# Performance work log

Hardware: AMD Instinct MI355X
Metric: run time of the kernel (lower is better)

## Reference

```python
import jax, jax.numpy as jnp
import numpy as np

NG, NPG, NF = 256, 64, 64          # graphs, nodes/graph, features (NPG == NF: x is per-graph [N,N])
HC, NL = 504, 4                     # hidden_channels, num_layers (HC*NL == TRIU)
E_PER = 1024                        # edges per graph
ALPHA = 0.5
EPS = 1e-5
TRIU = NF * (NF - 1) // 2           # 2016 strict-upper-triangle entries
HIDDEN, NCLS = 1024, 2


def _bn(x, g, b):
    # BatchNorm1d in training mode: biased batch statistics
    m = x.mean(0)
    v = x.var(0)
    return (x - m) * jax.lax.rsqrt(v + EPS) * g + b


def _gcn(x, src, dst, W, b):
    n = x.shape[0]
    xw = x @ W
    deg = jax.ops.segment_sum(jnp.ones(src.shape[0], x.dtype), dst, num_segments=n) + 1.0
    dinv = jax.lax.rsqrt(deg)
    coef = (dinv[src] * dinv[dst])[:, None]
    agg = jax.ops.segment_sum(xw[src] * coef, dst, num_segments=n)
    return agg + xw * (dinv * dinv)[:, None] + b


def _pool(x, batch):
    # global_mean_pool; every graph has exactly NPG nodes
    return jax.ops.segment_sum(x, batch, num_segments=NG) / NPG


def setup_inputs():
    key = jax.random.key(0)
    ks = jax.random.split(key, 16)
    total = NG * NPG
    x = jax.random.normal(ks[0], (total, NF), jnp.float32)
    offs = (jnp.arange(NG) * NPG)[:, None]
    edge_src = (jax.random.randint(ks[1], (NG, E_PER), 0, NPG) + offs).reshape(-1)
    edge_dst = (jax.random.randint(ks[2], (NG, E_PER), 0, NPG) + offs).reshape(-1)
    batch = jnp.arange(total) // NPG

    def lin(k, fi, fo):
        return jax.random.normal(k, (fi, fo), jnp.float32) / np.sqrt(fi)

    Wg0 = lin(ks[3], NF, HC)
    bg0 = jnp.zeros((HC,), jnp.float32)
    Wg_rest = jax.random.normal(ks[4], (NL - 1, HC, HC), jnp.float32) / np.sqrt(HC)
    bg_rest = jnp.zeros((NL - 1, HC), jnp.float32)
    gx = jnp.ones((TRIU,), jnp.float32); bx = jnp.zeros((TRIU,), jnp.float32)
    gh = jnp.ones((HC * NL,), jnp.float32); bh = jnp.zeros((HC * NL,), jnp.float32)
    Watt = lin(ks[5], TRIU, 1); batt = jnp.zeros((1,), jnp.float32)
    D1 = TRIU + HC * NL  # 4032
    Wm1 = lin(ks[6], D1, HIDDEN); bm1 = jnp.zeros((HIDDEN,), jnp.float32)
    gm1 = jnp.ones((HIDDEN,), jnp.float32); bem1 = jnp.zeros((HIDDEN,), jnp.float32)
    Wm2 = lin(ks[7], HIDDEN, HIDDEN // 2); bm2 = jnp.zeros((HIDDEN // 2,), jnp.float32)
    gm2 = jnp.ones((HIDDEN // 2,), jnp.float32); bem2 = jnp.zeros((HIDDEN // 2,), jnp.float32)
    Wm3 = lin(ks[8], HIDDEN // 2, HIDDEN // 2); bm3 = jnp.zeros((HIDDEN // 2,), jnp.float32)
    gm3 = jnp.ones((HIDDEN // 2,), jnp.float32); bem3 = jnp.zeros((HIDDEN // 2,), jnp.float32)
    Wm4 = lin(ks[9], HIDDEN // 2, NCLS); bm4 = jnp.zeros((NCLS,), jnp.float32)
    return dict(x=x, Wg0=Wg0, bg0=bg0, Wg_rest=Wg_rest, bg_rest=bg_rest, gx=gx, bx=bx,
                gh=gh, bh=bh, Watt=Watt, batt=batt, Wm1=Wm1, bm1=bm1, gm1=gm1, bem1=bem1,
                Wm2=Wm2, bm2=bm2, gm2=gm2, bem2=bem2, Wm3=Wm3, bm3=bm3, gm3=gm3, bem3=bem3,
                Wm4=Wm4, bm4=bm4, edge_src=edge_src, edge_dst=edge_dst, batch=batch)


def reference(x, Wg0, bg0, Wg_rest, bg_rest, gx, bx, gh, bh, Watt, batt,
              Wm1, bm1, gm1, bem1, Wm2, bm2, gm2, bem2, Wm3, bm3, gm3, bem3,
              Wm4, bm4, edge_src, edge_dst, batch):
    # stacked GCN convs (no nonlinearity between convs, as in source)
    cur = _gcn(x, edge_src, edge_dst, Wg0, bg0)
    hs = [_pool(cur, batch)]
    for i in range(NL - 1):
        cur = _gcn(cur, edge_src, edge_dst, Wg_rest[i], bg_rest[i])
        hs.append(_pool(cur, batch))
    h = _bn(jnp.concatenate(hs, axis=1), gh, bh)          # [NG, HC*NL]
    # per-graph strict upper triangle of the [N,N] input matrix (== triu().nonzero() trick)
    iu, ju = jnp.triu_indices(NF, k=1)
    xv = x.reshape(NG, NPG, NF)[:, iu, ju]                # [NG, TRIU]
    xv = _bn(xv, gx, bx)
    att = jax.nn.sigmoid(xv @ Watt + batt)                # [NG, 1]
    xf = att * xv + (1.0 - att) * h * ALPHA               # attention-weighted fusion
    z = jnp.concatenate([xf, h], axis=1)                  # [NG, TRIU + HC*NL]
    z = jax.nn.relu(_bn(z @ Wm1 + bm1, gm1, bem1))
    z = jax.nn.relu(_bn(z @ Wm2 + bm2, gm2, bem2))
    z = jax.nn.relu(_bn(z @ Wm3 + bm3, gm3, bem3))
    return z @ Wm4 + bm4                                   # [NG, NCLS]
```

## Files before the change

kernel.cpp:

```cpp
#include <hip/hip_runtime.h>
#include <math.h>

#define NGRAPH 256
#define NPG 64
#define NFEAT 64
#define HC 504
#define NLAY 4
#define EPER 1024
#define NTRIU 2016
#define DCAT 4032
#define HID1 1024
#define HID2 512

#define GCN_LDS (65536 + 73728 + 16384)

typedef __attribute__((ext_vector_type(8))) short bfrag8;
typedef __attribute__((ext_vector_type(4))) float f32x4;

struct __align__(8) us4 { unsigned short a, b, c, d; };

__device__ __forceinline__ unsigned short f2b(float f) {
    union { float f; unsigned u; } v; v.f = f;
    unsigned r = (v.u + 0x7fffu + ((v.u >> 16) & 1u)) >> 16;
    return (unsigned short)r;
}
__device__ __forceinline__ float b2f(unsigned short h) {
    union { unsigned u; float f; } v; v.u = ((unsigned)h) << 16;
    return v.f;
}

__global__ void triu_off(int* __restrict__ off)
{
    int i = threadIdx.x;
    if (i >= 63) return;
    int o = 63 * i - i * (i - 1) / 2;
    for (int j = i + 1; j < 64; ++j) { off[o] = i * 64 + j; ++o; }
}

__global__ void convWt(const float* __restrict__ W, unsigned short* __restrict__ Wt,
                       int K, int N, int KP, long long sStride, long long dStride)
{
    W  += (size_t)blockIdx.z * sStride;
    Wt += (size_t)blockIdx.z * dStride;
    __shared__ float T[32][33];
    int k0 = blockIdx.y * 32, n0 = blockIdx.x * 32;
    int tx = threadIdx.x, ty = threadIdx.y;
#pragma unroll
    for (int j = 0; j < 32; j += 8) {
        int k = k0 + ty + j, n = n0 + tx;
        T[ty + j][tx] = (k < K && n < N) ? W[(size_t)k * N + n] : 0.f;
    }
    __syncthreads();
#pragma unroll
    for (int j = 0; j < 32; j += 8) {
        int n = n0 + ty + j, k = k0 + tx;
        Wt[(size_t)n * KP + k] = f2b(T[tx][ty + j]);
    }
}

__global__ void convW4(const float* __restrict__ W, unsigned short* __restrict__ W4,
                       int K, int N, int KL, long long sStride, long long dStride)
{
    W  += (size_t)blockIdx.z * sStride;
    W4 += (size_t)blockIdx.z * dStride;
    __shared__ float T[32][33];
    int k0 = blockIdx.y * 32, n0 = blockIdx.x * 32;
    int tx = threadIdx.x, ty = threadIdx.y;
#pragma unroll
    for (int j = 0; j < 32; j += 8) {
        int k = k0 + ty + j, n = n0 + tx;
        T[ty + j][tx] = (k < K && n < N) ? W[(size_t)k * N + n] : 0.f;
    }
    __syncthreads();
#pragma unroll
    for (int j = 0; j < 32; j += 8) {
        int n = n0 + ty + j, k = k0 + tx;
        int idx = ((n >> 4) * (KL >> 5) + (k >> 5)) * 512
                + (((k >> 3) & 3) << 7) + ((n & 15) << 3) + (k & 7);
        W4[idx] = f2b(T[tx][ty + j]);
    }
}

template<int KL>
__device__ __forceinline__ void gcn_layer(const unsigned short* __restrict__ W4,
                                          const float* __restrict__ bias,
                                          unsigned short* cur, unsigned short* xwt,
                                          const unsigned short* ahl,
                                          float* __restrict__ hsg,
                                          int wv, int lm, int lh)
{
    constexpr int KTS = KL >> 5;
    const int colw = wv << 6;
    const int kswz = (lm & 7) << 3;
    const int lane8 = ((lh << 4) + lm) << 3;

    float bv[4];
#pragma unroll
    for (int cc = 0; cc < 4; ++cc) {
        int c = colw + cc * 16 + lm;
        bv[cc] = (c < HC) ? bias[c] : 0.f;
    }

    f32x4 acc[4][4];
#pragma unroll
    for (int m0 = 0; m0 < 4; ++m0)
#pragma unroll
        for (int cc = 0; cc < 4; ++cc) acc[m0][cc] = (f32x4){0.f, 0.f, 0.f, 0.f};

    bfrag8 bq[2][4];
#pragma unroll
    for (int cc = 0; cc < 4; ++cc)
        bq[0][cc] = *(const bfrag8*)(const void*)&W4[(size_t)((wv * 4 + cc) * KTS + 0) * 512 + lane8];
    if (KTS > 1) {
#pragma unroll
        for (int cc = 0; cc < 4; ++cc)
            bq[1][cc] = *(const bfrag8*)(const void*)&W4[(size_t)((wv * 4 + cc) * KTS + 1) * 512 + lane8];
    }
#pragma unroll
    for (int kt = 0; kt < KTS; ++kt) {
        bfrag8 a[4];
#pragma unroll
        for (int m0 = 0; m0 < 4; ++m0)
            a[m0] = *(const bfrag8*)(const void*)&cur[(m0 * 16 + lm) * 512 + ((kt * 32 + (lh << 3)) ^ kswz)];
        bfrag8 bc[4];
#pragma unroll
        for (int cc = 0; cc < 4; ++cc) bc[cc] = bq[kt & 1][cc];
        if (kt + 2 < KTS) {
#pragma unroll
            for (int cc = 0; cc < 4; ++cc)
                bq[kt & 1][cc] = *(const bfrag8*)(const void*)&W4[(size_t)((wv * 4 + cc) * KTS + kt + 2) * 512 + lane8];
        }
#pragma unroll
        for (int cc = 0; cc < 4; ++cc)
#pragma unroll
            for (int m0 = 0; m0 < 4; ++m0)
                acc[m0][cc] = __builtin_amdgcn_mfma_f32_16x16x32_bf16(a[m0], bc[cc], acc[m0][cc], 0, 0, 0);
    }
    __syncthreads();

#pragma unroll
    for (int cc = 0; cc < 4; ++cc) {
        const int c = colw + cc * 16 + lm;
#pragma unroll
        for (int m0 = 0; m0 < 4; ++m0) {
            const int rloc = m0 * 16 + (lh << 2);
            us4 p;
            p.a = f2b(acc[m0][cc][0]); p.b = f2b(acc[m0][cc][1]);
            p.c = f2b(acc[m0][cc][2]); p.d = f2b(acc[m0][cc][3]);
            *(us4*)(void*)&xwt[c * 72 + rloc] = p;
        }
    }

    bfrag8 ahf[4][2], alf[4][2];
#pragma unroll
    for (int m0 = 0; m0 < 4; ++m0)
#pragma unroll
        for (int kc = 0; kc < 2; ++kc) {
            int o = (m0 * 16 + lm) * 64 + kc * 32 + (lh << 3);
            ahf[m0][kc] = *(const bfrag8*)(const void*)&ahl[o];
            alf[m0][kc] = *(const bfrag8*)(const void*)&ahl[4096 + o];
        }
#pragma unroll
    for (int m0 = 0; m0 < 4; ++m0)
#pragma unroll
        for (int cc = 0; cc < 4; ++cc) acc[m0][cc] = (f32x4){0.f, 0.f, 0.f, 0.f};
#pragma unroll
    for (int cc = 0; cc < 4; ++cc) {
        const int c = colw + cc * 16 + lm;
        bfrag8 b0 = *(const bfrag8*)(const void*)&xwt[c * 72 + (lh << 3)];
        bfrag8 b1 = *(const bfrag8*)(const void*)&xwt[c * 72 + 32 + (lh << 3)];
#pragma unroll
        for (int m0 = 0; m0 < 4; ++m0) {
            acc[m0][cc] = __builtin_amdgcn_mfma_f32_16x16x32_bf16(ahf[m0][0], b0, acc[m0][cc], 0, 0, 0);
            acc[m0][cc] = __builtin_amdgcn_mfma_f32_16x16x32_bf16(alf[m0][0], b0, acc[m0][cc], 0, 0, 0);
            acc[m0][cc] = __builtin_amdgcn_mfma_f32_16x16x32_bf16(ahf[m0][1], b1, acc[m0][cc], 0, 0, 0);
            acc[m0][cc] = __builtin_amdgcn_mfma_f32_16x16x32_bf16(alf[m0][1], b1, acc[m0][cc], 0, 0, 0);
        }
    }

#pragma unroll
    for (int cc = 0; cc < 4; ++cc) {
        const int c = colw + cc * 16 + lm;
        float cs = 0.f;
#pragma unroll
        for (int m0 = 0; m0 < 4; ++m0) {
            const int rb = m0 * 16 + (lh << 2);
#pragma unroll
            for (int r = 0; r < 4; ++r) {
                float v = acc[m0][cc][r] + bv[cc];
                cs += v;
                const int row = rb + r;
                cur[row * 512 + (c ^ ((row & 7) << 3))] = f2b(v);
            }
        }
        cs += __shfl_xor(cs, 16, 64);
        cs += __shfl_xor(cs, 32, 64);
        if (lh == 0 && c < HC) hsg[c] = cs * (1.0f / 64.0f);
    }
    __syncthreads();
}

__global__ __launch_bounds__(512, 2) void gcn_all(const float* __restrict__ x,
                                                  const int* __restrict__ esrc,
                                                  const int* __restrict__ edst,
                                                  const unsigned short* __restrict__ Wt0,
                                                  const unsigned short* __restrict__ Wt123,
                                                  const float* __restrict__ bg0,
                                                  const float* __restrict__ bgR,
                                                  float* __restrict__ hs)
{
    extern __shared__ char lds[];
    unsigned short* cur = (unsigned short*)lds;
    unsigned short* xwt = (unsigned short*)(lds + 65536);
    unsigned short* ahl = (unsigned short*)(lds + 65536 + 73728);
    float* Af   = (float*)(lds + 65536);
    int*   cnt  = (int*)(lds + 65536 + 16384);
    float* dinv = (float*)(lds + 65536 + 16384 + 256);

    const int g = blockIdx.x, tid = threadIdx.x;
    const int wv = tid >> 6, lane = tid & 63;
    const int lm = lane & 15, lh = lane >> 4;

    for (int i = tid; i < 4096; i += 512) Af[i] = 0.f;
    if (tid < 64) cnt[tid] = 0;
    __syncthreads();
    for (int e = tid; e < EPER; e += 512)
        atomicAdd(&cnt[edst[(size_t)g * EPER + e] & 63], 1);
    __syncthreads();
    if (tid < 64) dinv[tid] = rsqrtf((float)cnt[tid] + 1.0f);
    __syncthreads();
    for (int e = tid; e < EPER; e += 512) {
        int s = esrc[(size_t)g * EPER + e] & 63;
        int d = edst[(size_t)g * EPER + e] & 63;
        atomicAdd(&Af[d * 64 + s], dinv[s] * dinv[d]);
    }
    __syncthreads();
    if (tid < 64) Af[tid * 64 + tid] += dinv[tid] * dinv[tid];
    __syncthreads();
    for (int i = tid; i < 4096; i += 512) {
        float v = Af[i];
        unsigned short h = f2b(v);
        ahl[i] = h;
        ahl[4096 + i] = f2b(v - b2f(h));
    }
    for (int i = tid; i < 1024; i += 512) {
        float4 v = ((const float4*)(x + (size_t)g * 4096))[i];
        int row = (i * 4) >> 6, col = (i * 4) & 63;
        unsigned short* p = &cur[row * 512 + (col ^ ((row & 7) << 3))];
        p[0] = f2b(v.x); p[1] = f2b(v.y); p[2] = f2b(v.z); p[3] = f2b(v.w);
    }
    __syncthreads();

    float* hsg = hs + (size_t)g * (HC * NLAY);
    gcn_layer<64>(Wt0, bg0, cur, xwt, ahl, hsg, wv, lm, lh);
    for (int l = 1; l < NLAY; ++l)
        gcn_layer<512>(Wt123 + (size_t)(l - 1) * 262144, bgR + (l - 1) * HC,
                       cur, xwt, ahl, hsg + l * HC, wv, lm, lh);
}

__global__ __launch_bounds__(256) void stats_part(const float* __restrict__ in,
                                                  float* __restrict__ ps,
                                                  float* __restrict__ pss,
                                                  int F, int rpb)
{
    int f = blockIdx.x * 256 + threadIdx.x;
    if (f >= F) return;
    int r0 = blockIdx.y * rpb;
    float s = 0.f, ss = 0.f;
    for (int r = r0; r < r0 + rpb; ++r) {
        float v = in[(size_t)r * F + f];
        s += v; ss += v * v;
    }
    ps [(size_t)blockIdx.y * F + f] = s;
    pss[(size_t)blockIdx.y * F + f] = ss;
}

__global__ __launch_bounds__(256) void stats_fin(const float* __restrict__ ps,
                                                 const float* __restrict__ pss,
                                                 float* __restrict__ mean,
                                                 float* __restrict__ inv,
                                                 int F, int GB, float invR)
{
    int f = blockIdx.x * 256 + threadIdx.x;
    if (f >= F) return;
    float s = 0.f, ss = 0.f;
    for (int b = 0; b < GB; ++b) { s += ps[(size_t)b * F + f]; ss += pss[(size_t)b * F + f]; }
    float m = s * invR;
    mean[f] = m;
    inv[f]  = rsqrtf(ss * invR - m * m + 1e-5f);
}

__global__ __launch_bounds__(256) void xv_gather(const float* __restrict__ x,
                                                 const int* __restrict__ off,
                                                 float* __restrict__ xv,
                                                 float* __restrict__ ps,
                                                 float* __restrict__ pss)
{
    int t = blockIdx.x * 256 + threadIdx.x;
    if (t >= NTRIU) return;
    int o = off[t];
    int g0 = blockIdx.y * 16;
    float s = 0.f, ss = 0.f;
    for (int g = g0; g < g0 + 16; ++g) {
        float v = x[(size_t)g * 4096 + o];
        xv[(size_t)g * NTRIU + t] = v;
        s += v; ss += v * v;
    }
    ps [(size_t)blockIdx.y * NTRIU + t] = s;
    pss[(size_t)blockIdx.y * NTRIU + t] = ss;
}

__global__ __launch_bounds__(256) void attz_fused(const float* __restrict__ xv,
                                                  const float* __restrict__ xm,
                                                  const float* __restrict__ xi,
                                                  const float* __restrict__ gx,
                                                  const float* __restrict__ bx,
                                                  const float* __restrict__ hsrc,
                                                  const float* __restrict__ hm,
                                                  const float* __restrict__ hi,
                                                  const float* __restrict__ gh,
                                                  const float* __restrict__ bh,
                                                  const float* __restrict__ Watt,
                                                  const float* __restrict__ batt,
                                                  unsigned short* __restrict__ zhi,
                                                  unsigned short* __restrict__ zlo)
{
    int g = blockIdx.x;
    __shared__ float xs[NTRIU];
    __shared__ float red[256];
    float s = 0.f;
    for (int t = threadIdx.x; t < NTRIU; t += 256) {
        float v = (xv[(size_t)g * NTRIU + t] - xm[t]) * xi[t] * gx[t] + bx[t];
        xs[t] = v;
        s += v * Watt[t];
    }
    red[threadIdx.x] = s;
    __syncthreads();
    for (int w = 128; w > 0; w >>= 1) {
        if (threadIdx.x < w) red[threadIdx.x] += red[threadIdx.x + w];
        __syncthreads();
    }
    float att = 1.0f / (1.0f + expf(-(red[0] + batt[0])));
    for (int t = threadIdx.x; t < NTRIU; t += 256) {
        float hn = (hsrc[(size_t)g * NTRIU + t] - hm[t]) * hi[t] * gh[t] + bh[t];
        float zf = att * xs[t] + (1.0f - att) * hn * 0.5f;
        unsigned short h0 = f2b(zf);
        zhi[(size_t)g * DCAT + t] = h0;
        zlo[(size_t)g * DCAT + t] = f2b(zf - b2f(h0));
        unsigned short h1 = f2b(hn);
        zhi[(size_t)g * DCAT + NTRIU + t] = h1;
        zlo[(size_t)g * DCAT + NTRIU + t] = f2b(hn - b2f(h1));
    }
}

__global__ __launch_bounds__(256) void gemm_bf_sk(const unsigned short* __restrict__ Ahi,
                                                  const unsigned short* __restrict__ Alo,
                                                  const unsigned short* __restrict__ Bt,
                                                  float* __restrict__ P,
                                                  int N, int K, int chunk)
{
    __shared__ unsigned short Ah[2][2048], Al[2][2048], Bs[2][2048];
    const int tid  = threadIdx.x;
    const int wave = tid >> 6, lane = tid & 63;
    const int row0 = blockIdx.y << 6, col0 = blockIdx.x << 6;
    const int kb = blockIdx.z * chunk;
    const int NT = chunk >> 5;
    const int sr = tid >> 2, sk = (tid & 3) << 3;
    const unsigned short* gAh = Ahi + (size_t)(row0 + sr) * K + kb + sk;
    const unsigned short* gAl = Alo + (size_t)(row0 + sr) * K + kb + sk;
    const unsigned short* gB  = Bt  + (size_t)(col0 + sr) * K + kb + sk;

    int4 rh = *(const int4*)(const void*)gAh;
    int4 rl = *(const int4*)(const void*)gAl;
    int4 rb = *(const int4*)(const void*)gB;
    *(int4*)(void*)&Ah[0][tid << 3] = rh;
    *(int4*)(void*)&Al[0][tid << 3] = rl;
    *(int4*)(void*)&Bs[0][tid << 3] = rb;
    __syncthreads();

    f32x4 acc0 = {0.f, 0.f, 0.f, 0.f};
    f32x4 acc1 = acc0, acc2 = acc0, acc3 = acc0;
    const int aoff = (wave * 16 + (lane & 15)) * 32 + ((lane >> 4) << 3);
    const int boff = (lane & 15) * 32 + ((lane >> 4) << 3);

    for (int t = 0; t < NT; ++t) {
        if (t + 1 < NT) {
            rh = *(const int4*)(const void*)(gAh + (t + 1) * 32);
            rl = *(const int4*)(const void*)(gAl + (t + 1) * 32);
            rb = *(const int4*)(const void*)(gB  + (t + 1) * 32);
        }
        const unsigned short* ah = Ah[t & 1];
        const unsigned short* al = Al[t & 1];
        const unsigned short* bs = Bs[t & 1];
        bfrag8 a  = *(const bfrag8*)(const void*)&ah[aoff];
        bfrag8 a2 = *(const bfrag8*)(const void*)&al[aoff];
        bfrag8 b0 = *(const bfrag8*)(const void*)&bs[boff];
        bfrag8 b1 = *(const bfrag8*)(const void*)&bs[boff + 16 * 32];
        bfrag8 b2 = *(const bfrag8*)(const void*)&bs[boff + 32 * 32];
        bfrag8 b3 = *(const bfrag8*)(const void*)&bs[boff + 48 * 32];
        acc0 = __builtin_amdgcn_mfma_f32_16x16x32_bf16(a,  b0, acc0, 0, 0, 0);
        acc0 = __builtin_amdgcn_mfma_f32_16x16x32_bf16(a2, b0, acc0, 0, 0, 0);
        acc1 = __builtin_amdgcn_mfma_f32_16x16x32_bf16(a,  b1, acc1, 0, 0, 0);
        acc1 = __builtin_amdgcn_mfma_f32_16x16x32_bf16(a2, b1, acc1, 0, 0, 0);
        acc2 = __builtin_amdgcn_mfma_f32_16x16x32_bf16(a,  b2, acc2, 0, 0, 0);
        acc2 = __builtin_amdgcn_mfma_f32_16x16x32_bf16(a2, b2, acc2, 0, 0, 0);
        acc3 = __builtin_amdgcn_mfma_f32_16x16x32_bf16(a,  b3, acc3, 0, 0, 0);
        acc3 = __builtin_amdgcn_mfma_f32_16x16x32_bf16(a2, b3, acc3, 0, 0, 0);
        if (t + 1 < NT) {
            *(int4*)(void*)&Ah[(t + 1) & 1][tid << 3] = rh;
            *(int4*)(void*)&Al[(t + 1) & 1][tid << 3] = rl;
            *(int4*)(void*)&Bs[(t + 1) & 1][tid << 3] = rb;
        }
        __syncthreads();
    }

    float* Pp = P + (size_t)blockIdx.z * NGRAPH * N;
    const int rbase = row0 + wave * 16 + ((lane >> 4) << 2);
    const int cbase = col0 + (lane & 15);
#pragma unroll
    for (int r = 0; r < 4; ++r) {
        int grow = rbase + r;
        Pp[(size_t)grow * N + cbase +  0] = acc0[r];
        Pp[(size_t)grow * N + cbase + 16] = acc1[r];
        Pp[(size_t)grow * N + cbase + 32] = acc2[r];
        Pp[(size_t)grow * N + cbase + 48] = acc3[r];
    }
}

__global__ __launch_bounds__(256) void reduce_add(const float* __restrict__ P,
                                                  const float* __restrict__ bias,
                                                  float* __restrict__ C, int MN,
                                                  int Nmask, int S)
{
    int i = blockIdx.x * 256 + threadIdx.x;
    if (i >= MN) return;
    float s = 0.f;
    for (int t = 0; t < S; ++t) s += P[(size_t)t * MN + i];
    C[i] = s + bias[i & Nmask];
}

__global__ __launch_bounds__(256) void bn_apply_bf(const float* __restrict__ M_,
                                                   const float* __restrict__ mean,
                                                   const float* __restrict__ inv,
                                                   const float* __restrict__ gamma,
                                                   const float* __restrict__ beta,
                                                   unsigned short* __restrict__ hi,
                                                   unsigned short* __restrict__ lo,
                                                   int total, int mask)
{
    int i = blockIdx.x * 256 + threadIdx.x;
    if (i >= total) return;
    int f = i & mask;
    float v = (M_[i] - mean[f]) * inv[f] * gamma[f] + beta[f];
    v = fmaxf(v, 0.f);
    unsigned short h = f2b(v);
    hi[i] = h;
    lo[i] = f2b(v - b2f(h));
}

__global__ __launch_bounds__(256) void final_kernel(const unsigned short* __restrict__ Xhi,
                                                    const unsigned short* __restrict__ Xlo,
                                                    const float* __restrict__ W,
                                                    const float* __restrict__ b,
                                                    float* __restrict__ out)
{
    int g = blockIdx.x;
    float s0 = 0.f, s1 = 0.f;
    for (int k = threadIdx.x; k < HID2; k += 256) {
        float v = b2f(Xhi[(size_t)g * HID2 + k]) + b2f(Xlo[(size_t)g * HID2 + k]);
        s0 += v * W[k * 2 + 0];
        s1 += v * W[k * 2 + 1];
    }
    __shared__ float r0[256], r1[256];
    r0[threadIdx.x] = s0; r1[threadIdx.x] = s1;
    __syncthreads();
    for (int w = 128; w > 0; w >>= 1) {
        if (threadIdx.x < w) {
            r0[threadIdx.x] += r0[threadIdx.x + w];
            r1[threadIdx.x] += r1[threadIdx.x + w];
        }
        __syncthreads();
    }
    if (threadIdx.x == 0) {
        out[g * 2 + 0] = r0[0] + b[0];
        out[g * 2 + 1] = r1[0] + b[1];
    }
}

extern "C" void kernel_launch(void* const* d_in, const int* in_sizes, int n_in,
                              void* d_out, int out_size, void* d_ws, size_t ws_size,
                              hipStream_t stream)
{
    const float* x      = (const float*)d_in[0];
    const float* Wg0    = (const float*)d_in[1];
    const float* bg0    = (const float*)d_in[2];
    const float* WgR    = (const float*)d_in[3];
    const float* bgR    = (const float*)d_in[4];
    const float* gx     = (const float*)d_in[5];
    const float* bx     = (const float*)d_in[6];
    const float* gh     = (const float*)d_in[7];
    const float* bh     = (const float*)d_in[8];
    const float* Watt   = (const float*)d_in[9];
    const float* batt   = (const float*)d_in[10];
    const float* Wm1    = (const float*)d_in[11];
    const float* bm1    = (const float*)d_in[12];
    const float* gm1    = (const float*)d_in[13];
    const float* bem1   = (const float*)d_in[14];
    const float* Wm2    = (const float*)d_in[15];
    const float* bm2    = (const float*)d_in[16];
    const float* gm2    = (const float*)d_in[17];
    const float* bem2   = (const float*)d_in[18];
    const float* Wm3    = (const float*)d_in[19];
    const float* bm3    = (const float*)d_in[20];
    const float* gm3    = (const float*)d_in[21];
    const float* bem3   = (const float*)d_in[22];
    const float* Wm4    = (const float*)d_in[23];
    const float* bm4    = (const float*)d_in[24];
    const int*   esrc   = (const int*)d_in[25];
    const int*   edst   = (const int*)d_in[26];
    float* out = (float*)d_out;

    char* w = (char*)d_ws;
    auto alloc = [&](size_t bytes) -> char* {
        char* p = w;
        w += (bytes + 255) & ~(size_t)255;
        return p;
    };
    unsigned short* Wt0   = (unsigned short*)alloc((size_t)512 * 64 * 2);
    unsigned short* Wt123 = (unsigned short*)alloc((size_t)3 * 512 * 512 * 2);
    unsigned short* W1t   = (unsigned short*)alloc((size_t)HID1 * DCAT * 2);
    unsigned short* W2t   = (unsigned short*)alloc((size_t)HID2 * HID1 * 2);
    unsigned short* W3t   = (unsigned short*)alloc((size_t)HID2 * HID2 * 2);
    float*          hs    = (float*)alloc((size_t)NGRAPH * NTRIU * 4);
    float*          xv    = (float*)alloc((size_t)NGRAPH * NTRIU * 4);
    unsigned short* zhi   = (unsigned short*)alloc((size_t)NGRAPH * DCAT * 2);
    unsigned short* zlo   = (unsigned short*)alloc((size_t)NGRAPH * DCAT * 2);
    float*          P     = (float*)alloc((size_t)8 * NGRAPH * HID1 * 4);
    float*          mf    = (float*)alloc((size_t)NGRAPH * HID1 * 4);
    unsigned short* m1hi  = (unsigned short*)alloc((size_t)NGRAPH * HID1 * 2);
    unsigned short* m1lo  = (unsigned short*)alloc((size_t)NGRAPH * HID1 * 2);
    unsigned short* m2hi  = (unsigned short*)alloc((size_t)NGRAPH * HID2 * 2);
    unsigned short* m2lo  = (unsigned short*)alloc((size_t)NGRAPH * HID2 * 2);
    unsigned short* m3hi  = (unsigned short*)alloc((size_t)NGRAPH * HID2 * 2);
    unsigned short* m3lo  = (unsigned short*)alloc((size_t)NGRAPH * HID2 * 2);
    float*          ps    = (float*)alloc((size_t)16 * NTRIU * 4);
    float*          pss   = (float*)alloc((size_t)16 * NTRIU * 4);
    float*          xm    = (float*)alloc(NTRIU * 4);
    float*          xi    = (float*)alloc(NTRIU * 4);
    float*          hm    = (float*)alloc(NTRIU * 4);
    float*          hiv   = (float*)alloc(NTRIU * 4);
    float*          mmean = (float*)alloc(HID1 * 4);
    float*          minv  = (float*)alloc(HID1 * 4);
    int*            off   = (int*)alloc(NTRIU * 4);

    hipFuncSetAttribute((const void*)gcn_all,
                        hipFuncAttributeMaxDynamicSharedMemorySize, GCN_LDS);

    triu_off<<<1, 64, 0, stream>>>(off);
    convW4<<<dim3(16, 2, 1),   dim3(32, 8), 0, stream>>>(Wg0, Wt0, 64, HC, 64, 0, 0);
    convW4<<<dim3(16, 16, 3),  dim3(32, 8), 0, stream>>>(WgR, Wt123, HC, HC, 512,
                                                         (long long)HC * HC, 512LL * 512);
    convWt<<<dim3(32, 126, 1), dim3(32, 8), 0, stream>>>(Wm1, W1t, DCAT, HID1, DCAT, 0, 0);
    convWt<<<dim3(16, 32, 1),  dim3(32, 8), 0, stream>>>(Wm2, W2t, HID1, HID2, HID1, 0, 0);
    convWt<<<dim3(16, 16, 1),  dim3(32, 8), 0, stream>>>(Wm3, W3t, HID2, HID2, HID2, 0, 0);

    gcn_all<<<NGRAPH, 512, GCN_LDS, stream>>>(x, esrc, edst, Wt0, Wt123, bg0, bgR, hs);

    stats_part<<<dim3(8, 16), 256, 0, stream>>>(hs, ps, pss, NTRIU, 16);
    stats_fin<<<8, 256, 0, stream>>>(ps, pss, hm, hiv, NTRIU, 16, 1.0f / NGRAPH);
    xv_gather<<<dim3(8, 16), 256, 0, stream>>>(x, off, xv, ps, pss);
    stats_fin<<<8, 256, 0, stream>>>(ps, pss, xm, xi, NTRIU, 16, 1.0f / NGRAPH);
    attz_fused<<<NGRAPH, 256, 0, stream>>>(xv, xm, xi, gx, bx, hs, hm, hiv, gh, bh,
                                           Watt, batt, zhi, zlo);

    gemm_bf_sk<<<dim3(16, 4, 7), 256, 0, stream>>>(zhi, zlo, W1t, P, HID1, DCAT, 576);
    reduce_add<<<1024, 256, 0, stream>>>(P, bm1, mf, NGRAPH * HID1, HID1 - 1, 7);
    stats_part<<<dim3(4, 16), 256, 0, stream>>>(mf, ps, pss, HID1, 16);
    stats_fin<<<4, 256, 0, stream>>>(ps, pss, mmean, minv, HID1, 16, 1.0f / NGRAPH);
    bn_apply_bf<<<1024, 256, 0, stream>>>(mf, mmean, minv, gm1, bem1, m1hi, m1lo,
                                          NGRAPH * HID1, HID1 - 1);

    gemm_bf_sk<<<dim3(8, 4, 8), 256, 0, stream>>>(m1hi, m1lo, W2t, P, HID2, HID1, 128);
    reduce_add<<<512, 256, 0, stream>>>(P, bm2, mf, NGRAPH * HID2, HID2 - 1, 8);
    stats_part<<<dim3(2, 16), 256, 0, stream>>>(mf, ps, pss, HID2, 16);
    stats_fin<<<2, 256, 0, stream>>>(ps, pss, mmean, minv, HID2, 16, 1.0f / NGRAPH);
    bn_apply_bf<<<512, 256, 0, stream>>>(mf, mmean, minv, gm2, bem2, m2hi, m2lo,
                                         NGRAPH * HID2, HID2 - 1);

    gemm_bf_sk<<<dim3(8, 4, 8), 256, 0, stream>>>(m2hi, m2lo, W3t, P, HID2, HID2, 64);
    reduce_add<<<512, 256, 0, stream>>>(P, bm3, mf, NGRAPH * HID2, HID2 - 1, 8);
    stats_part<<<dim3(2, 16), 256, 0, stream>>>(mf, ps, pss, HID2, 16);
    stats_fin<<<2, 256, 0, stream>>>(ps, pss, mmean, minv, HID2, 16, 1.0f / NGRAPH);
    bn_apply_bf<<<512, 256, 0, stream>>>(mf, mmean, minv, gm3, bem3, m3hi, m3lo,
                                         NGRAPH * HID2, HID2 - 1);

    final_kernel<<<NGRAPH, 256, 0, stream>>>(m3hi, m3lo, Wm4, bm4, out);
}
```

Measured before the change: 175.9 us.

## Widen GCN block to 1024 threads, fuse split-K reduce with BN stats, drop triu kernel

The per-graph GCN kernel now runs 1024 threads (16 waves), each owning 32 output columns instead of 64. The aggregation GEMM is transposed so results are written to LDS as packed 4-wide stores, and pooled sums are reduced with shuffles and float4 writes. Separately, the split-K reduction is fused with the BatchNorm partial-statistics pass, which removes one kernel and one read of the intermediate per MLP layer. The triu offset kernel is replaced by closed-form index math inside xv_gather. The wider block halves the per-wave register footprint but adds more waves competing for LDS and barriers, and the fused reduce uses fewer, larger blocks.

```diff
diff --git a/kernel.cpp b/kernel.cpp
--- a/kernel.cpp
+++ b/kernel.cpp
@@ -29,14 +29,6 @@
     return v.f;
 }
 
-__global__ void triu_off(int* __restrict__ off)
-{
-    int i = threadIdx.x;
-    if (i >= 63) return;
-    int o = 63 * i - i * (i - 1) / 2;
-    for (int j = i + 1; j < 64; ++j) { off[o] = i * 64 + j; ++o; }
-}
-
 __global__ void convWt(const float* __restrict__ W, unsigned short* __restrict__ Wt,
                        int K, int N, int KP, long long sStride, long long dStride)
 {
@@ -90,31 +82,24 @@
                                           int wv, int lm, int lh)
 {
     constexpr int KTS = KL >> 5;
-    const int colw = wv << 6;
+    const int colw = wv << 5;
     const int kswz = (lm & 7) << 3;
     const int lane8 = ((lh << 4) + lm) << 3;
 
-    float bv[4];
-#pragma unroll
-    for (int cc = 0; cc < 4; ++cc) {
-        int c = colw + cc * 16 + lm;
-        bv[cc] = (c < HC) ? bias[c] : 0.f;
-    }
-
-    f32x4 acc[4][4];
+    f32x4 acc[4][2];
 #pragma unroll
     for (int m0 = 0; m0 < 4; ++m0)
 #pragma unroll
-        for (int cc = 0; cc < 4; ++cc) acc[m0][cc] = (f32x4){0.f, 0.f, 0.f, 0.f};
-
-    bfrag8 bq[2][4];
-#pragma unroll
-    for (int cc = 0; cc < 4; ++cc)
-        bq[0][cc] = *(const bfrag8*)(const void*)&W4[(size_t)((wv * 4 + cc) * KTS + 0) * 512 + lane8];
+        for (int cc = 0; cc < 2; ++cc) acc[m0][cc] = (f32x4){0.f, 0.f, 0.f, 0.f};
+
+    bfrag8 bq[2][2];
+#pragma unroll
+    for (int cc = 0; cc < 2; ++cc)
+        bq[0][cc] = *(const bfrag8*)(const void*)&W4[(size_t)((wv * 2 + cc) * KTS + 0) * 512 + lane8];
     if (KTS > 1) {
 #pragma unroll
-        for (int cc = 0; cc < 4; ++cc)
-            bq[1][cc] = *(const bfrag8*)(const void*)&W4[(size_t)((wv * 4 + cc) * KTS + 1) * 512 + lane8];
+        for (int cc = 0; cc < 2; ++cc)
+            bq[1][cc] = *(const bfrag8*)(const void*)&W4[(size_t)((wv * 2 + cc) * KTS + 1) * 512 + lane8];
     }
 #pragma unroll
     for (int kt = 0; kt < KTS; ++kt) {
@@ -122,16 +107,15 @@
 #pragma unroll
         for (int m0 = 0; m0 < 4; ++m0)
             a[m0] = *(const bfrag8*)(const void*)&cur[(m0 * 16 + lm) * 512 + ((kt * 32 + (lh << 3)) ^ kswz)];
-        bfrag8 bc[4];
-#pragma unroll
-        for (int cc = 0; cc < 4; ++cc) bc[cc] = bq[kt & 1][cc];
+        bfrag8 bc[2];
+        bc[0] = bq[kt & 1][0]; bc[1] = bq[kt & 1][1];
         if (kt + 2 < KTS) {
 #pragma unroll
-            for (int cc = 0; cc < 4; ++cc)
-                bq[kt & 1][cc] = *(const bfrag8*)(const void*)&W4[(size_t)((wv * 4 + cc) * KTS + kt + 2) * 512 + lane8];
-        }
-#pragma unroll
-        for (int cc = 0; cc < 4; ++cc)
+            for (int cc = 0; cc < 2; ++cc)
+                bq[kt & 1][cc] = *(const bfrag8*)(const void*)&W4[(size_t)((wv * 2 + cc) * KTS + kt + 2) * 512 + lane8];
+        }
+#pragma unroll
+        for (int cc = 0; cc < 2; ++cc)
 #pragma unroll
             for (int m0 = 0; m0 < 4; ++m0)
                 acc[m0][cc] = __builtin_amdgcn_mfma_f32_16x16x32_bf16(a[m0], bc[cc], acc[m0][cc], 0, 0, 0);
@@ -139,75 +123,85 @@
     __syncthreads();
 
 #pragma unroll
-    for (int cc = 0; cc < 4; ++cc) {
+    for (int cc = 0; cc < 2; ++cc) {
         const int c = colw + cc * 16 + lm;
 #pragma unroll
         for (int m0 = 0; m0 < 4; ++m0) {
-            const int rloc = m0 * 16 + (lh << 2);
             us4 p;
             p.a = f2b(acc[m0][cc][0]); p.b = f2b(acc[m0][cc][1]);
             p.c = f2b(acc[m0][cc][2]); p.d = f2b(acc[m0][cc][3]);
-            *(us4*)(void*)&xwt[c * 72 + rloc] = p;
-        }
-    }
-
-    bfrag8 ahf[4][2], alf[4][2];
-#pragma unroll
-    for (int m0 = 0; m0 < 4; ++m0)
-#pragma unroll
-        for (int kc = 0; kc < 2; ++kc) {
-            int o = (m0 * 16 + lm) * 64 + kc * 32 + (lh << 3);
-            ahf[m0][kc] = *(const bfrag8*)(const void*)&ahl[o];
-            alf[m0][kc] = *(const bfrag8*)(const void*)&ahl[4096 + o];
-        }
-#pragma unroll
-    for (int m0 = 0; m0 < 4; ++m0)
-#pragma unroll
-        for (int cc = 0; cc < 4; ++cc) acc[m0][cc] = (f32x4){0.f, 0.f, 0.f, 0.f};
-#pragma unroll
-    for (int cc = 0; cc < 4; ++cc) {
-        const int c = colw + cc * 16 + lm;
-        bfrag8 b0 = *(const bfrag8*)(const void*)&xwt[c * 72 + (lh << 3)];
-        bfrag8 b1 = *(const bfrag8*)(const void*)&xwt[c * 72 + 32 + (lh << 3)];
-#pragma unroll
-        for (int m0 = 0; m0 < 4; ++m0) {
-            acc[m0][cc] = __builtin_amdgcn_mfma_f32_16x16x32_bf16(ahf[m0][0], b0, acc[m0][cc], 0, 0, 0);
-            acc[m0][cc] = __builtin_amdgcn_mfma_f32_16x16x32_bf16(alf[m0][0], b0, acc[m0][cc], 0, 0, 0);
-            acc[m0][cc] = __builtin_amdgcn_mfma_f32_16x16x32_bf16(ahf[m0][1], b1, acc[m0][cc], 0, 0, 0);
-            acc[m0][cc] = __builtin_amdgcn_mfma_f32_16x16x32_bf16(alf[m0][1], b1, acc[m0][cc], 0, 0, 0);
-        }
-    }
-
-#pragma unroll
-    for (int cc = 0; cc < 4; ++cc) {
-        const int c = colw + cc * 16 + lm;
-        float cs = 0.f;
-#pragma unroll
-        for (int m0 = 0; m0 < 4; ++m0) {
-            const int rb = m0 * 16 + (lh << 2);
-#pragma unroll
-            for (int r = 0; r < 4; ++r) {
-                float v = acc[m0][cc][r] + bv[cc];
-                cs += v;
-                const int row = rb + r;
-                cur[row * 512 + (c ^ ((row & 7) << 3))] = f2b(v);
-            }
-        }
-        cs += __shfl_xor(cs, 16, 64);
-        cs += __shfl_xor(cs, 32, 64);
-        if (lh == 0 && c < HC) hsg[c] = cs * (1.0f / 64.0f);
-    }
-    __syncthreads();
-}
-
-__global__ __launch_bounds__(512, 2) void gcn_all(const float* __restrict__ x,
-                                                  const int* __restrict__ esrc,
-                                                  const int* __restrict__ edst,
-                                                  const unsigned short* __restrict__ Wt0,
-                                                  const unsigned short* __restrict__ Wt123,
-                                                  const float* __restrict__ bg0,
-                                                  const float* __restrict__ bgR,
-                                                  float* __restrict__ hs)
+            *(us4*)(void*)&xwt[c * 72 + m0 * 16 + (lh << 2)] = p;
+        }
+    }
+
+    f32x4 acc2[2][4];
+#pragma unroll
+    for (int cc = 0; cc < 2; ++cc)
+#pragma unroll
+        for (int n0 = 0; n0 < 4; ++n0) acc2[cc][n0] = (f32x4){0.f, 0.f, 0.f, 0.f};
+#pragma unroll
+    for (int n0 = 0; n0 < 4; ++n0) {
+        const int o = (n0 * 16 + lm) * 64 + (lh << 3);
+        bfrag8 bh0 = *(const bfrag8*)(const void*)&ahl[o];
+        bfrag8 bh1 = *(const bfrag8*)(const void*)&ahl[o + 32];
+        bfrag8 bl0 = *(const bfrag8*)(const void*)&ahl[4096 + o];
+        bfrag8 bl1 = *(const bfrag8*)(const void*)&ahl[4096 + o + 32];
+#pragma unroll
+        for (int cc = 0; cc < 2; ++cc) {
+            const int c = colw + cc * 16 + lm;
+            bfrag8 a0 = *(const bfrag8*)(const void*)&xwt[c * 72 + (lh << 3)];
+            bfrag8 a1 = *(const bfrag8*)(const void*)&xwt[c * 72 + 32 + (lh << 3)];
+            acc2[cc][n0] = __builtin_amdgcn_mfma_f32_16x16x32_bf16(a0, bh0, acc2[cc][n0], 0, 0, 0);
+            acc2[cc][n0] = __builtin_amdgcn_mfma_f32_16x16x32_bf16(a0, bl0, acc2[cc][n0], 0, 0, 0);
+            acc2[cc][n0] = __builtin_amdgcn_mfma_f32_16x16x32_bf16(a1, bh1, acc2[cc][n0], 0, 0, 0);
+            acc2[cc][n0] = __builtin_amdgcn_mfma_f32_16x16x32_bf16(a1, bl1, acc2[cc][n0], 0, 0, 0);
+        }
+    }
+
+#pragma unroll
+    for (int cc = 0; cc < 2; ++cc) {
+        const int cb = colw + cc * 16 + (lh << 2);
+        float bv[4];
+#pragma unroll
+        for (int r = 0; r < 4; ++r) {
+            int c = cb + r;
+            bv[r] = (c < HC) ? bias[c] : 0.f;
+        }
+        float t0 = 0.f, t1 = 0.f, t2 = 0.f, t3 = 0.f;
+#pragma unroll
+        for (int n0 = 0; n0 < 4; ++n0) {
+            const int d = n0 * 16 + lm;
+            float v0 = acc2[cc][n0][0] + bv[0];
+            float v1 = acc2[cc][n0][1] + bv[1];
+            float v2 = acc2[cc][n0][2] + bv[2];
+            float v3 = acc2[cc][n0][3] + bv[3];
+            t0 += v0; t1 += v1; t2 += v2; t3 += v3;
+            us4 p;
+            p.a = f2b(v0); p.b = f2b(v1); p.c = f2b(v2); p.d = f2b(v3);
+            *(us4*)(void*)&cur[d * 512 + (cb ^ ((d & 7) << 3))] = p;
+        }
+#pragma unroll
+        for (int m = 1; m < 16; m <<= 1) {
+            t0 += __shfl_xor(t0, m, 64);
+            t1 += __shfl_xor(t1, m, 64);
+            t2 += __shfl_xor(t2, m, 64);
+            t3 += __shfl_xor(t3, m, 64);
+        }
+        if (lm == 0 && cb < HC)
+            *(float4*)&hsg[cb] = make_float4(t0 * (1.0f / 64.0f), t1 * (1.0f / 64.0f),
+                                             t2 * (1.0f / 64.0f), t3 * (1.0f / 64.0f));
+    }
+    __syncthreads();
+}
+
+__global__ __launch_bounds__(1024, 4) void gcn_all(const float* __restrict__ x,
+                                                   const int* __restrict__ esrc,
+                                                   const int* __restrict__ edst,
+                                                   const unsigned short* __restrict__ Wt0,
+                                                   const unsigned short* __restrict__ Wt123,
+                                                   const float* __restrict__ bg0,
+                                                   const float* __restrict__ bgR,
+                                                   float* __restrict__ hs)
 {
     extern __shared__ char lds[];
     unsigned short* cur = (unsigned short*)lds;
@@ -221,31 +215,30 @@
     const int wv = tid >> 6, lane = tid & 63;
     const int lm = lane & 15, lh = lane >> 4;
 
-    for (int i = tid; i < 4096; i += 512) Af[i] = 0.f;
+    for (int i = tid; i < 4096; i += 1024) Af[i] = 0.f;
     if (tid < 64) cnt[tid] = 0;
     __syncthreads();
-    for (int e = tid; e < EPER; e += 512)
-        atomicAdd(&cnt[edst[(size_t)g * EPER + e] & 63], 1);
+    atomicAdd(&cnt[edst[(size_t)g * EPER + tid] & 63], 1);
     __syncthreads();
     if (tid < 64) dinv[tid] = rsqrtf((float)cnt[tid] + 1.0f);
     __syncthreads();
-    for (int e = tid; e < EPER; e += 512) {
-        int s = esrc[(size_t)g * EPER + e] & 63;
-        int d = edst[(size_t)g * EPER + e] & 63;
+    {
+        int s = esrc[(size_t)g * EPER + tid] & 63;
+        int d = edst[(size_t)g * EPER + tid] & 63;
         atomicAdd(&Af[d * 64 + s], dinv[s] * dinv[d]);
     }
     __syncthreads();
     if (tid < 64) Af[tid * 64 + tid] += dinv[tid] * dinv[tid];
     __syncthreads();
-    for (int i = tid; i < 4096; i += 512) {
+    for (int i = tid; i < 4096; i += 1024) {
         float v = Af[i];
         unsigned short h = f2b(v);
         ahl[i] = h;
         ahl[4096 + i] = f2b(v - b2f(h));
     }
-    for (int i = tid; i < 1024; i += 512) {
-        float4 v = ((const float4*)(x + (size_t)g * 4096))[i];
-        int row = (i * 4) >> 6, col = (i * 4) & 63;
+    {
+        float4 v = ((const float4*)(x + (size_t)g * 4096))[tid];
+        int row = (tid * 4) >> 6, col = (tid * 4) & 63;
         unsigned short* p = &cur[row * 512 + (col ^ ((row & 7) << 3))];
         p[0] = f2b(v.x); p[1] = f2b(v.y); p[2] = f2b(v.z); p[3] = f2b(v.w);
     }
@@ -291,14 +284,17 @@
 }
 
 __global__ __launch_bounds__(256) void xv_gather(const float* __restrict__ x,
-                                                 const int* __restrict__ off,
                                                  float* __restrict__ xv,
                                                  float* __restrict__ ps,
                                                  float* __restrict__ pss)
 {
     int t = blockIdx.x * 256 + threadIdx.x;
     if (t >= NTRIU) return;
-    int o = off[t];
+    int i = (int)(63.5f - sqrtf(63.5f * 63.5f - 2.0f * (float)t));
+    while (63 * (i + 1) - (i + 1) * i / 2 <= t) ++i;
+    while (63 * i - i * (i - 1) / 2 > t) --i;
+    int j = t - (63 * i - i * (i - 1) / 2) + i + 1;
+    int o = i * 64 + j;
     int g0 = blockIdx.y * 16;
     float s = 0.f, ss = 0.f;
     for (int g = g0; g < g0 + 16; ++g) {
@@ -427,16 +423,27 @@
     }
 }
 
-__global__ __launch_bounds__(256) void reduce_add(const float* __restrict__ P,
-                                                  const float* __restrict__ bias,
-                                                  float* __restrict__ C, int MN,
-                                                  int Nmask, int S)
-{
-    int i = blockIdx.x * 256 + threadIdx.x;
-    if (i >= MN) return;
-    float s = 0.f;
-    for (int t = 0; t < S; ++t) s += P[(size_t)t * MN + i];
-    C[i] = s + bias[i & Nmask];
+__global__ __launch_bounds__(256) void reduce_stats(const float* __restrict__ P,
+                                                    const float* __restrict__ bias,
+                                                    float* __restrict__ mf,
+                                                    float* __restrict__ ps,
+                                                    float* __restrict__ pss,
+                                                    int N, int S)
+{
+    int f = blockIdx.x * 256 + threadIdx.x;
+    int r0 = blockIdx.y * 8;
+    size_t MN = (size_t)NGRAPH * N;
+    float bv = bias[f];
+    float s = 0.f, ss = 0.f;
+    for (int r = r0; r < r0 + 8; ++r) {
+        float v = 0.f;
+        for (int t = 0; t < S; ++t) v += P[(size_t)t * MN + (size_t)r * N + f];
+        v += bv;
+        mf[(size_t)r * N + f] = v;
+        s += v; ss += v * v;
+    }
+    ps [(size_t)blockIdx.y * N + f] = s;
+    pss[(size_t)blockIdx.y * N + f] = ss;
 }
 
 __global__ __launch_bounds__(256) void bn_apply_bf(const float* __restrict__ M_,
@@ -543,20 +550,18 @@
     unsigned short* m2lo  = (unsigned short*)alloc((size_t)NGRAPH * HID2 * 2);
     unsigned short* m3hi  = (unsigned short*)alloc((size_t)NGRAPH * HID2 * 2);
     unsigned short* m3lo  = (unsigned short*)alloc((size_t)NGRAPH * HID2 * 2);
-    float*          ps    = (float*)alloc((size_t)16 * NTRIU * 4);
-    float*          pss   = (float*)alloc((size_t)16 * NTRIU * 4);
+    float*          ps    = (float*)alloc((size_t)32 * NTRIU * 4);
+    float*          pss   = (float*)alloc((size_t)32 * NTRIU * 4);
     float*          xm    = (float*)alloc(NTRIU * 4);
     float*          xi    = (float*)alloc(NTRIU * 4);
     float*          hm    = (float*)alloc(NTRIU * 4);
     float*          hiv   = (float*)alloc(NTRIU * 4);
     float*          mmean = (float*)alloc(HID1 * 4);
     float*          minv  = (float*)alloc(HID1 * 4);
-    int*            off   = (int*)alloc(NTRIU * 4);
 
     hipFuncSetAttribute((const void*)gcn_all,
                         hipFuncAttributeMaxDynamicSharedMemorySize, GCN_LDS);
 
-    triu_off<<<1, 64, 0, stream>>>(off);
     convW4<<<dim3(16, 2, 1),   dim3(32, 8), 0, stream>>>(Wg0, Wt0, 64, HC, 64, 0, 0);
     convW4<<<dim3(16, 16, 3),  dim3(32, 8), 0, stream>>>(WgR, Wt123, HC, HC, 512,
                                                          (long long)HC * HC, 512LL * 512);
@@ -564,33 +569,30 @@
     convWt<<<dim3(16, 32, 1),  dim3(32, 8), 0, stream>>>(Wm2, W2t, HID1, HID2, HID1, 0, 0);
     convWt<<<dim3(16, 16, 1),  dim3(32, 8), 0, stream>>>(Wm3, W3t, HID2, HID2, HID2, 0, 0);
 
-    gcn_all<<<NGRAPH, 512, GCN_LDS, stream>>>(x, esrc, edst, Wt0, Wt123, bg0, bgR, hs);
+    gcn_all<<<NGRAPH, 1024, GCN_LDS, stream>>>(x, esrc, edst, Wt0, Wt123, bg0, bgR, hs);
 
     stats_part<<<dim3(8, 16), 256, 0, stream>>>(hs, ps, pss, NTRIU, 16);
     stats_fin<<<8, 256, 0, stream>>>(ps, pss, hm, hiv, NTRIU, 16, 1.0f / NGRAPH);
-    xv_gather<<<dim3(8, 16), 256, 0, stream>>>(x, off, xv, ps, pss);
+    xv_gather<<<dim3(8, 16), 256, 0, stream>>>(x, xv, ps, pss);
     stats_fin<<<8, 256, 0, stream>>>(ps, pss, xm, xi, NTRIU, 16, 1.0f / NGRAPH);
     attz_fused<<<NGRAPH, 256, 0, stream>>>(xv, xm, xi, gx, bx, hs, hm, hiv, gh, bh,
                                            Watt, batt, zhi, zlo);
 
     gemm_bf_sk<<<dim3(16, 4, 7), 256, 0, stream>>>(zhi, zlo, W1t, P, HID1, DCAT, 576);
-    reduce_add<<<1024, 256, 0, stream>>>(P, bm1, mf, NGRAPH * HID1, HID1 - 1, 7);
-    stats_part<<<dim3(4, 16), 256, 0, stream>>>(mf, ps, pss, HID1, 16);
-    stats_fin<<<4, 256, 0, stream>>>(ps, pss, mmean, minv, HID1, 16, 1.0f / NGRAPH);
+    reduce_stats<<<dim3(4, 32), 256, 0, stream>>>(P, bm1, mf, ps, pss, HID1, 7);
+    stats_fin<<<4, 256, 0, stream>>>(ps, pss, mmean, minv, HID1, 32, 1.0f / NGRAPH);
     bn_apply_bf<<<1024, 256, 0, stream>>>(mf, mmean, minv, gm1, bem1, m1hi, m1lo,
                                           NGRAPH * HID1, HID1 - 1);
 
     gemm_bf_sk<<<dim3(8, 4, 8), 256, 0, stream>>>(m1hi, m1lo, W2t, P, HID2, HID1, 128);
-    reduce_add<<<512, 256, 0, stream>>>(P, bm2, mf, NGRAPH * HID2, HID2 - 1, 8);
-    stats_part<<<dim3(2, 16), 256, 0, stream>>>(mf, ps, pss, HID2, 16);
-    stats_fin<<<2, 256, 0, stream>>>(ps, pss, mmean, minv, HID2, 16, 1.0f / NGRAPH);
+    reduce_stats<<<dim3(2, 32), 256, 0, stream>>>(P, bm2, mf, ps, pss, HID2, 8);
+    stats_fin<<<2, 256, 0, stream>>>(ps, pss, mmean, minv, HID2, 32, 1.0f / NGRAPH);
     bn_apply_bf<<<512, 256, 0, stream>>>(mf, mmean, minv, gm2, bem2, m2hi, m2lo,
                                          NGRAPH * HID2, HID2 - 1);
 
     gemm_bf_sk<<<dim3(8, 4, 8), 256, 0, stream>>>(m2hi, m2lo, W3t, P, HID2, HID2, 64);
-    reduce_add<<<512, 256, 0, stream>>>(P, bm3, mf, NGRAPH * HID2, HID2 - 1, 8);
-    stats_part<<<dim3(2, 16), 256, 0, stream>>>(mf, ps, pss, HID2, 16);
-    stats_fin<<<2, 256, 0, stream>>>(ps, pss, mmean, minv, HID2, 16, 1.0f / NGRAPH);
+    reduce_stats<<<dim3(2, 32), 256, 0, stream>>>(P, bm3, mf, ps, pss, HID2, 8);
+    stats_fin<<<2, 256, 0, stream>>>(ps, pss, mmean, minv, HID2, 32, 1.0f / NGRAPH);
     bn_apply_bf<<<512, 256, 0, stream>>>(mf, mmean, minv, gm3, bem3, m3hi, m3lo,
                                          NGRAPH * HID2, HID2 - 1);
 
```

New measurement: 203.3 us. 1.16x slower.
